# Optimization experiments

Hardware: AMD Instinct MI355X
Metric: run time of the kernel (lower is better)

## Reference

```python
import jax, jax.numpy as jnp
import numpy as np

N_NODES = 100000
N_EDGES = 1600000
N_GRAPHS = 1024
DIM_IN = 128
DIM_SF = 32
DIM_OUT = 8
EPS = 1e-5


def setup_inputs() -> dict:
    key = jax.random.key(0)
    ks = jax.random.split(key, 16)
    feat = jax.random.normal(ks[0], (N_NODES, DIM_IN), dtype=jnp.float32)
    self_feat = jax.random.normal(ks[1], (N_GRAPHS, DIM_SF), dtype=jnp.float32)
    src = jax.random.randint(ks[2], (N_EDGES,), 0, N_NODES)
    dst = jax.random.randint(ks[3], (N_EDGES,), 0, N_NODES)
    node2graph = jnp.sort(jax.random.randint(ks[4], (N_NODES,), 0, N_GRAPHS))

    def lin(k, din, dout):
        s = 1.0 / np.sqrt(din)
        kw, kb = jax.random.split(k)
        W = jax.random.uniform(kw, (din, dout), minval=-s, maxval=s, dtype=jnp.float32)
        b = jax.random.uniform(kb, (dout,), minval=-s, maxval=s, dtype=jnp.float32)
        return W, b

    W1, b1 = lin(ks[5], DIM_IN, 100)
    W2, b2 = lin(ks[6], 100, 20)
    Wf1, bf1 = lin(ks[7], 20 * DIM_SF, 128)
    Wf2, bf2 = lin(ks[8], 128, 32)
    Wf3, bf3 = lin(ks[9], 32, DIM_OUT)
    g1 = jnp.ones((128,), jnp.float32); be1 = jnp.zeros((128,), jnp.float32)
    g2 = jnp.ones((32,), jnp.float32); be2 = jnp.zeros((32,), jnp.float32)
    return dict(feat=feat, self_feat=self_feat, src=src, dst=dst,
                node2graph=node2graph, W1=W1, b1=b1, W2=W2, b2=b2,
                Wf1=Wf1, bf1=bf1, g1=g1, be1=be1,
                Wf2=Wf2, bf2=bf2, g2=g2, be2=be2, Wf3=Wf3, bf3=bf3)


def _gcn_layer(h, src, dst, W, b):
    # copy_u + mean reduce: segment-mean of source features onto destinations.
    n = h.shape[0]
    msum = jax.ops.segment_sum(h[src], dst, num_segments=n)        # [N, d]
    deg = jax.ops.segment_sum(jnp.ones((src.shape[0], 1), h.dtype), dst,
                              num_segments=n)                      # [N, 1]
    # DGL: nodes with no incoming messages keep their previous 'h'.
    agg = jnp.where(deg > 0, msum / jnp.maximum(deg, 1.0), h)
    return agg @ W + b


def _bn(x, gamma, beta):
    # BatchNorm1d in training mode: biased batch statistics.
    mu = jnp.mean(x, axis=0)
    var = jnp.mean((x - mu) ** 2, axis=0)
    return (x - mu) / jnp.sqrt(var + EPS) * gamma + beta


def reference(feat, self_feat, src, dst, node2graph,
              W1, b1, W2, b2, Wf1, bf1, g1, be1, Wf2, bf2, g2, be2, Wf3, bf3):
    h = jax.nn.relu(_gcn_layer(feat, src, dst, W1, b1))            # [N, 100]
    h = jax.nn.relu(_gcn_layer(h, src, dst, W2, b2))               # [N, 20]
    # dgl.mean_nodes: per-graph mean pooling
    hsum = jax.ops.segment_sum(h, node2graph, num_segments=N_GRAPHS)
    cnt = jax.ops.segment_sum(jnp.ones((h.shape[0], 1), h.dtype), node2graph,
                              num_segments=N_GRAPHS)
    hg = hsum / jnp.maximum(cnt, 1.0)                              # [G, 20]
    # Kronecker fusion: bmm(hg[:, :, None], self_feat[:, None, :])
    fused = (hg[:, :, None] * self_feat[:, None, :]).reshape(hg.shape[0], -1)
    out = jax.nn.relu(_bn(fused @ Wf1 + bf1, g1, be1))
    out = jax.nn.relu(_bn(out @ Wf2 + bf2, g2, be2))
    return out @ Wf3 + bf3                                         # [G, 8]
```

## Files before the change

### kernel.cpp

```cpp
#include <hip/hip_runtime.h>
#include <hip/hip_fp16.h>

#define N_NODES 100000
#define N_EDGES 1600000
#define N_GRAPHS 1024
#define DIM_IN 128
#define D1 100
#define D1P 128
#define D2 20
#define D2P 32
#define DIM_SF 32
#define DF1 128
#define DF2 32
#define DOUT 8
#define EPS 1e-5f
#define NPW 8

typedef _Float16 hh2 __attribute__((ext_vector_type(2)));

__device__ __forceinline__ void fdacc(unsigned u, float& lo, float& hi) {
  const hh2 MLO = {(_Float16)1.0f, (_Float16)0.0f};
  const hh2 MHI = {(_Float16)0.0f, (_Float16)1.0f};
  hh2 h = __builtin_bit_cast(hh2, u);
  lo = __builtin_amdgcn_fdot2(h, MLO, lo, false);
  hi = __builtin_amdgcn_fdot2(h, MHI, hi, false);
}

__device__ __forceinline__ unsigned pkadd(unsigned a, unsigned b) {
  __half2 x = __builtin_bit_cast(__half2, a);
  __half2 y = __builtin_bit_cast(__half2, b);
  return __builtin_bit_cast(unsigned, __hadd2(x, y));
}

#define NBK 512
#define BW 196
#define EPB 4096
#define NBLK1 ((N_EDGES + EPB - 1) / EPB)
#define GEMM1_NB (N_NODES / 80)

__global__ void __launch_bounds__(256) k_goff(const int* __restrict__ n2g,
                                              int* __restrict__ g_off,
                                              int* __restrict__ bucket_cnt) {
  int g = blockIdx.x * 256 + threadIdx.x;
  if (g < NBK) bucket_cnt[g] = 0;
  if (g > N_GRAPHS) return;
  if (g == N_GRAPHS) { g_off[g] = N_NODES; return; }
  int lo = 0, hi = N_NODES;
  while (lo < hi) {
    int mid = (lo + hi) >> 1;
    if (n2g[mid] < g) lo = mid + 1; else hi = mid;
  }
  g_off[g] = lo;
}

__global__ void __launch_bounds__(256) k_sc_gemm(const int* __restrict__ src,
                                                 const int* __restrict__ dst,
                                                 int* __restrict__ bucket_cnt,
                                                 unsigned* __restrict__ packed_out,
                                                 const float* __restrict__ feat,
                                                 const float* __restrict__ W1,
                                                 __half* __restrict__ p1h) {
  __shared__ __align__(16) char smem[31744];
  int t = threadIdx.x;
  if (blockIdx.x < NBLK1) {
    int* hist   = (int*)smem;
    int* lbase  = (int*)(smem + 2048);
    int* gbase  = (int*)(smem + 4096);
    int* ssum   = (int*)(smem + 6144);
    unsigned* sval = (unsigned*)(smem + 7168);
    unsigned short* sbkt = (unsigned short*)(smem + 23552);
    int blk = blockIdx.x;
    for (int i = t; i < NBK; i += 256) hist[i] = 0;
    __syncthreads();
    int base = blk * EPB;
    unsigned pk[16]; int bn[16]; int rk[16];
#pragma unroll
    for (int r = 0; r < 16; r++) {
      int e = base + r * 256 + t;
      bn[r] = -1;
      if (e < N_EDGES) {
        int dv = dst[e];
        unsigned b = (unsigned)dv / BW;
        unsigned ld = (unsigned)dv - b * BW;
        bn[r] = (int)b;
        pk[r] = ((unsigned)src[e] << 8) | ld;
        rk[r] = atomicAdd(&hist[b], 1);
      }
    }
    __syncthreads();
    int h0 = hist[2 * t], h1 = hist[2 * t + 1];
    int s = h0 + h1;
    ssum[t] = s; __syncthreads();
    for (int off = 1; off < 256; off <<= 1) {
      int x = (t >= off) ? ssum[t - off] : 0;
      __syncthreads();
      ssum[t] += x;
      __syncthreads();
    }
    int excl = ssum[t] - s;
    lbase[2 * t] = excl;
    lbase[2 * t + 1] = excl + h0;
    gbase[2 * t]     = (h0 > 0) ? (2 * t) * EPB     + atomicAdd(&bucket_cnt[2 * t],     h0) : 0;
    gbase[2 * t + 1] = (h1 > 0) ? (2 * t + 1) * EPB + atomicAdd(&bucket_cnt[2 * t + 1], h1) : 0;
    __syncthreads();
#pragma unroll
    for (int r = 0; r < 16; r++) {
      if (bn[r] >= 0) {
        int li = lbase[bn[r]] + rk[r];
        sval[li] = pk[r];
        sbkt[li] = (unsigned short)bn[r];
      }
    }
    __syncthreads();
    int cnt = N_EDGES - base; if (cnt > EPB) cnt = EPB;
    for (int i = t; i < cnt; i += 256) {
      int b = sbkt[i];
      packed_out[gbase[b] + (i - lbase[b])] = sval[i];
    }
  } else {
    float* w1s = (float*)smem;
    bool act = (t < 250);
    int q = t % 25, ng = t / 25;
    int n0 = (int)(blockIdx.x - NBLK1) * 80 + ng * 8;
    int c0 = q * 4;
    float acc[8][4] = {{0.f}};
    const float* f0 = feat + (size_t)n0 * DIM_IN;
    for (int pass = 0; pass < 2; pass++) {
      __syncthreads();
      for (int i = t; i < 64 * D1; i += 256) w1s[i] = W1[pass * 64 * D1 + i];
      __syncthreads();
      if (act) {
        int kg0 = pass * 64;
        for (int k = 0; k < 64; k += 4) {
          float4 w0 = *(const float4*)&w1s[(k + 0) * D1 + c0];
          float4 w1 = *(const float4*)&w1s[(k + 1) * D1 + c0];
          float4 w2 = *(const float4*)&w1s[(k + 2) * D1 + c0];
          float4 w3 = *(const float4*)&w1s[(k + 3) * D1 + c0];
#pragma unroll
          for (int j = 0; j < 8; j++) {
            float4 f = *(const float4*)(f0 + j * DIM_IN + kg0 + k);
            acc[j][0] += f.x * w0.x + f.y * w1.x + f.z * w2.x + f.w * w3.x;
            acc[j][1] += f.x * w0.y + f.y * w1.y + f.z * w2.y + f.w * w3.y;
            acc[j][2] += f.x * w0.z + f.y * w1.z + f.z * w2.z + f.w * w3.z;
            acc[j][3] += f.x * w0.w + f.y * w1.w + f.z * w2.w + f.w * w3.w;
          }
        }
      }
    }
    if (act) {
#pragma unroll
      for (int j = 0; j < 8; j++) {
        __half2* d2 = (__half2*)(p1h + (size_t)(n0 + j) * D1P + c0);
        d2[0] = __floats2half2_rn(acc[j][0], acc[j][1]);
        d2[1] = __floats2half2_rn(acc[j][2], acc[j][3]);
      }
    }
  }
}

__global__ void __launch_bounds__(256) k_bfine(const unsigned* __restrict__ packed_in,
                                               const int* __restrict__ bucket_cnt,
                                               int* __restrict__ csr,
                                               int* __restrict__ deg,
                                               int* __restrict__ row_off) {
  __shared__ unsigned sval[EPB];
  __shared__ int scsr[EPB];
  __shared__ int hist[256];
  __shared__ int soff[256];
  __shared__ int cur[256];
  int b = blockIdx.x, t = threadIdx.x;
  int start = b * EPB;
  int cnt = bucket_cnt[b];
  if (cnt > EPB) cnt = EPB;
  hist[t] = 0;
  __syncthreads();
  for (int i = t; i < cnt; i += 256) {
    unsigned v = packed_in[start + i];
    sval[i] = v;
    atomicAdd(&hist[v & 255u], 1);
  }
  __syncthreads();
  int h = hist[t];
  soff[t] = h; __syncthreads();
  for (int off = 1; off < 256; off <<= 1) {
    int x = (t >= off) ? soff[t - off] : 0;
    __syncthreads();
    soff[t] += x;
    __syncthreads();
  }
  int excl = soff[t] - h;
  cur[t] = excl;
  int n = b * BW + t;
  if (t < BW && n < N_NODES) { deg[n] = h; row_off[n] = start + excl; }
  __syncthreads();
  for (int i = t; i < cnt; i += 256) {
    unsigned v = sval[i];
    int pos = atomicAdd(&cur[v & 255u], 1);
    scsr[pos] = (int)(v >> 8);
  }
  __syncthreads();
  for (int i = t; i < cnt; i += 256) csr[start + i] = scsr[i];
}

__device__ __forceinline__ void acc8d(uint4 r, float4& A, float4& B) {
  fdacc(r.x, A.x, A.y);
  fdacc(r.y, A.z, A.w);
  fdacc(r.z, B.x, B.y);
  fdacc(r.w, B.z, B.w);
}

__global__ void __launch_bounds__(256) k_agg1(const __half* __restrict__ p1h,
                                              const int* __restrict__ deg,
                                              const int* __restrict__ row_off,
                                              const int* __restrict__ csr,
                                              const float* __restrict__ b1,
                                              const float* __restrict__ W2,
                                              __half* __restrict__ p2h) {
  __shared__ float w2s[D1 * D2];
  __shared__ float b1s[D1];
  __shared__ float hbuf[4][104];
  int t = threadIdx.x;
  for (int i = t; i < D1 * D2; i += 256) w2s[i] = W2[i];
  if (t < D1) b1s[t] = b1[t];
  __syncthreads();
  int w = t >> 6, lane = t & 63;
  int g = lane >> 4, o = lane & 15;
  const size_t oh = (size_t)(o * 8);
  int p = lane / 20;
  int j20 = lane - p * 20;
  int cbeg = (p == 0) ? 0 : (p == 1) ? 33 : 66;
  int cend = (p == 0) ? 33 : (p == 1) ? 66 : 100;
  if (p >= 3) { cbeg = 0; cend = 0; }
  int n0 = (blockIdx.x * 4 + w) * NPW;
  for (int nn = 0; nn < NPW; nn++) {
    int n = n0 + nn;
    int d = deg[n], ro = row_off[n];
    float4 A = {0.f, 0.f, 0.f, 0.f}, B = {0.f, 0.f, 0.f, 0.f};
    if (d > 0) {
      for (int base = 0; base < d; base += 64) {
        int m = d - base; if (m > 64) m = 64;
        int sv = (lane < m) ? csr[ro + base + lane] : 0;
        int nr = m >> 2;
        int r = 0;
        for (; r + 3 < nr; r += 4) {
          int sA = __shfl(sv, r * 4 + g);
          int sB = __shfl(sv, r * 4 + 4 + g);
          int sC = __shfl(sv, r * 4 + 8 + g);
          int sD = __shfl(sv, r * 4 + 12 + g);
          uint4 ra = *(const uint4*)(p1h + (size_t)sA * D1P + oh);
          uint4 rb = *(const uint4*)(p1h + (size_t)sB * D1P + oh);
          uint4 rc = *(const uint4*)(p1h + (size_t)sC * D1P + oh);
          uint4 rd = *(const uint4*)(p1h + (size_t)sD * D1P + oh);
          uint4 u, v2;
          u.x = pkadd(ra.x, rb.x); u.y = pkadd(ra.y, rb.y);
          u.z = pkadd(ra.z, rb.z); u.w = pkadd(ra.w, rb.w);
          v2.x = pkadd(rc.x, rd.x); v2.y = pkadd(rc.y, rd.y);
          v2.z = pkadd(rc.z, rd.z); v2.w = pkadd(rc.w, rd.w);
          acc8d(u, A, B);
          acc8d(v2, A, B);
        }
        if (r + 1 < nr) {
          int sA = __shfl(sv, r * 4 + g);
          int sB = __shfl(sv, r * 4 + 4 + g);
          uint4 ra = *(const uint4*)(p1h + (size_t)sA * D1P + oh);
          uint4 rb = *(const uint4*)(p1h + (size_t)sB * D1P + oh);
          uint4 u;
          u.x = pkadd(ra.x, rb.x); u.y = pkadd(ra.y, rb.y);
          u.z = pkadd(ra.z, rb.z); u.w = pkadd(ra.w, rb.w);
          acc8d(u, A, B);
          r += 2;
        }
        if (r < nr) {
          int sA = __shfl(sv, r * 4 + g);
          uint4 ra = *(const uint4*)(p1h + (size_t)sA * D1P + oh);
          acc8d(ra, A, B);
        }
        int rem = m & 3;
        int sT = __shfl(sv, nr * 4 + g);
        if (rem && g < rem) {
          uint4 ra = *(const uint4*)(p1h + (size_t)sT * D1P + oh);
          acc8d(ra, A, B);
        }
      }
    } else {
      if (g == 0) {
        uint4 ra = *(const uint4*)(p1h + (size_t)n * D1P + oh);
        acc8d(ra, A, B);
      }
    }
    float v[8] = {A.x, A.y, A.z, A.w, B.x, B.y, B.z, B.w};
#pragma unroll
    for (int j = 0; j < 8; j++) {
      v[j] += __shfl_down(v[j], 32);
      v[j] += __shfl_down(v[j], 16);
    }
    if (lane < 13) {
      float inv = (d > 0) ? 1.0f / (float)d : 1.0f;
#pragma unroll
      for (int j = 0; j < 8; j++) {
        int ch = 8 * lane + j;
        if (ch < D1) hbuf[w][ch] = fmaxf(v[j] * inv + b1s[ch], 0.f);
      }
    }
    float acc = 0.f;
    for (int c = cbeg; c < cend; c++) acc += hbuf[w][c] * w2s[c * D2 + j20];
    float t1 = __shfl_down(acc, 20);
    float t2 = __shfl_down(acc, 40);
    acc += t1 + t2;
    if (lane < D2)       p2h[(size_t)n * D2P + lane] = __float2half_rn(acc);
    else if (lane < D2P) p2h[(size_t)n * D2P + lane] = __float2half_rn(0.f);
  }
}

__global__ void __launch_bounds__(512) k_agg2(const __half* __restrict__ p2h,
                                              const int* __restrict__ deg,
                                              const int* __restrict__ row_off,
                                              const int* __restrict__ csr,
                                              const float* __restrict__ b2,
                                              const int* __restrict__ g_off,
                                              float* __restrict__ hg) {
  __shared__ float ssum[D2];
  __shared__ float b2s[D2];
  int t = threadIdx.x, w = t >> 6, lane = t & 63;
  int g = blockIdx.x;
  if (t < D2) { ssum[t] = 0.f; b2s[t] = b2[t]; }
  __syncthreads();
  const unsigned* pu = (const unsigned*)p2h;
  int n_lo = g_off[g], n_hi = g_off[g + 1];
  int nn = n_hi - n_lo;
  int e16 = lane >> 2, o = lane & 3;
  bool xtra = (o == 0);
  float4 GA = {0.f, 0.f, 0.f, 0.f};
  float4 GX = {0.f, 0.f, 0.f, 0.f};
  for (int n = n_lo + w; n < n_hi; n += 8) {
    int d = deg[n], ro = row_off[n];
    float4 A = {0.f, 0.f, 0.f, 0.f};
    float4 X = {0.f, 0.f, 0.f, 0.f};
    if (d > 0) {
      for (int base = 0; base < d; base += 64) {
        int m = d - base; if (m > 64) m = 64;
        int sv = (lane < m) ? csr[ro + base + lane] : 0;
        int nr = (m + 15) >> 4;
        for (int r = 0; r < nr; r++) {
          int ei = r * 16 + e16;
          int s0 = __shfl(sv, ei);
          if (ei < m) {
            const unsigned* row = pu + (size_t)s0 * 16;
            uint2 ra = *(const uint2*)(row + 2 * o);
            fdacc(ra.x, A.x, A.y);
            fdacc(ra.y, A.z, A.w);
            if (xtra) {
              uint2 rx = *(const uint2*)(row + 8);
              fdacc(rx.x, X.x, X.y);
              fdacc(rx.y, X.z, X.w);
            }
          }
        }
      }
    } else {
      if (e16 == 0) {
        const unsigned* row = pu + (size_t)n * 16;
        uint2 ra = *(const uint2*)(row + 2 * o);
        fdacc(ra.x, A.x, A.y);
        fdacc(ra.y, A.z, A.w);
        if (xtra) {
          uint2 rx = *(const uint2*)(row + 8);
          fdacc(rx.x, X.x, X.y);
          fdacc(rx.y, X.z, X.w);
        }
      }
    }
#pragma unroll
    for (int sft = 32; sft >= 4; sft >>= 1) {
      A.x += __shfl_down(A.x, sft); A.y += __shfl_down(A.y, sft);
      A.z += __shfl_down(A.z, sft); A.w += __shfl_down(A.w, sft);
      X.x += __shfl_down(X.x, sft); X.y += __shfl_down(X.y, sft);
      X.z += __shfl_down(X.z, sft); X.w += __shfl_down(X.w, sft);
    }
    float inv = (d > 0) ? 1.0f / (float)d : 1.0f;
    if (lane < 4) {
      int ch = 4 * lane;
      GA.x += fmaxf(A.x * inv + b2s[ch + 0], 0.f);
      GA.y += fmaxf(A.y * inv + b2s[ch + 1], 0.f);
      GA.z += fmaxf(A.z * inv + b2s[ch + 2], 0.f);
      GA.w += fmaxf(A.w * inv + b2s[ch + 3], 0.f);
      if (lane == 0) {
        GX.x += fmaxf(X.x * inv + b2s[16], 0.f);
        GX.y += fmaxf(X.y * inv + b2s[17], 0.f);
        GX.z += fmaxf(X.z * inv + b2s[18], 0.f);
        GX.w += fmaxf(X.w * inv + b2s[19], 0.f);
      }
    }
  }
  if (lane < 4) {
    int ch = 4 * lane;
    atomicAdd(&ssum[ch + 0], GA.x);
    atomicAdd(&ssum[ch + 1], GA.y);
    atomicAdd(&ssum[ch + 2], GA.z);
    atomicAdd(&ssum[ch + 3], GA.w);
    if (lane == 0) {
      atomicAdd(&ssum[16], GX.x);
      atomicAdd(&ssum[17], GX.y);
      atomicAdd(&ssum[18], GX.z);
      atomicAdd(&ssum[19], GX.w);
    }
  }
  __syncthreads();
  if (t < D2) {
    float inv = (nn > 0) ? 1.0f / (float)nn : 0.f;
    hg[g * D2 + t] = ssum[t] * inv;
  }
}

__global__ void __launch_bounds__(128) k_mlp1(const float* __restrict__ hg,
                                              const float* __restrict__ sf,
                                              const float* __restrict__ Wf1,
                                              const float* __restrict__ bf1,
                                              float* __restrict__ y1) {
  __shared__ float prod[D2 * DIM_SF];
  __shared__ float hgl[D2], sfl[DIM_SF];
  int g = blockIdx.x, t = threadIdx.x;
  if (t < D2) hgl[t] = hg[g * D2 + t];
  if (t < DIM_SF) sfl[t] = sf[g * DIM_SF + t];
  __syncthreads();
  for (int i = t; i < D2 * DIM_SF; i += 128) prod[i] = hgl[i >> 5] * sfl[i & 31];
  __syncthreads();
  float acc = bf1[t];
#pragma unroll 4
  for (int k = 0; k < D2 * DIM_SF; k++) acc += prod[k] * Wf1[k * DF1 + t];
  y1[g * DF1 + t] = acc;
}

__global__ void k_bnstats(const float* __restrict__ x, int ld,
                          float* __restrict__ mu, float* __restrict__ rstd) {
  __shared__ float ssum[256], ssq[256];
  int c = blockIdx.x, t = threadIdx.x;
  float s = 0.f, q = 0.f;
  for (int r = t; r < N_GRAPHS; r += 256) { float v = x[r * ld + c]; s += v; q += v * v; }
  ssum[t] = s; ssq[t] = q; __syncthreads();
  for (int off = 128; off > 0; off >>= 1) {
    if (t < off) { ssum[t] += ssum[t + off]; ssq[t] += ssq[t + off]; }
    __syncthreads();
  }
  if (t == 0) {
    float m = ssum[0] / (float)N_GRAPHS;
    float var = ssq[0] / (float)N_GRAPHS - m * m;
    mu[c] = m;
    rstd[c] = rsqrtf(var + EPS);
  }
}

__global__ void k_mlp2(const float* __restrict__ y1, const float* __restrict__ mu1,
                       const float* __restrict__ rstd1, const float* __restrict__ g1,
                       const float* __restrict__ be1, const float* __restrict__ Wf2,
                       const float* __restrict__ bf2, float* __restrict__ y2) {
  int idx = blockIdx.x * 256 + threadIdx.x;
  int g = idx >> 5, o = idx & 31;
  float acc = bf2[o];
  for (int k = 0; k < DF1; k++) {
    float x = (y1[g * DF1 + k] - mu1[k]) * rstd1[k] * g1[k] + be1[k];
    x = fmaxf(x, 0.f);
    acc += x * Wf2[k * DF2 + o];
  }
  y2[g * DF2 + o] = acc;
}

__global__ void k_mlp3(const float* __restrict__ y2, const float* __restrict__ mu2,
                       const float* __restrict__ rstd2, const float* __restrict__ g2,
                       const float* __restrict__ be2, const float* __restrict__ Wf3,
                       const float* __restrict__ bf3, float* __restrict__ out) {
  int idx = blockIdx.x * 256 + threadIdx.x;
  int g = idx >> 3, o = idx & 7;
  float acc = bf3[o];
  for (int k = 0; k < DF2; k++) {
    float x = (y2[g * DF2 + k] - mu2[k]) * rstd2[k] * g2[k] + be2[k];
    x = fmaxf(x, 0.f);
    acc += x * Wf3[k * DOUT + o];
  }
  out[g * DOUT + o] = acc;
}

extern "C" void kernel_launch(void* const* d_in, const int* in_sizes, int n_in,
                              void* d_out, int out_size, void* d_ws, size_t ws_size,
                              hipStream_t stream) {
  const float* feat = (const float*)d_in[0];
  const float* sf   = (const float*)d_in[1];
  const int*   src  = (const int*)d_in[2];
  const int*   dst  = (const int*)d_in[3];
  const int*   n2g  = (const int*)d_in[4];
  const float* W1   = (const float*)d_in[5];
  const float* b1   = (const float*)d_in[6];
  const float* W2   = (const float*)d_in[7];
  const float* b2   = (const float*)d_in[8];
  const float* Wf1  = (const float*)d_in[9];
  const float* bf1  = (const float*)d_in[10];
  const float* g1   = (const float*)d_in[11];
  const float* be1  = (const float*)d_in[12];
  const float* Wf2  = (const float*)d_in[13];
  const float* bf2  = (const float*)d_in[14];
  const float* g2   = (const float*)d_in[15];
  const float* be2  = (const float*)d_in[16];
  const float* Wf3  = (const float*)d_in[17];
  const float* bf3  = (const float*)d_in[18];
  float* out = (float*)d_out;

  char* ws = (char*)d_ws;
  size_t off = 0;
  auto alloc = [&](size_t bytes) -> void* {
    void* p = ws + off;
    off = (off + bytes + 255) & ~(size_t)255;
    return p;
  };
  int*      bucket_cnt = (int*)alloc(NBK * 4);
  int*      g_offs   = (int*)alloc((N_GRAPHS + 1) * 4);
  float*    hg       = (float*)alloc(N_GRAPHS * D2 * 4);
  int*      deg      = (int*)alloc(N_NODES * 4);
  int*      row_off  = (int*)alloc(N_NODES * 4);
  unsigned* packed   = (unsigned*)alloc((size_t)NBK * EPB * 4);
  int*      csr      = (int*)alloc((size_t)NBK * EPB * 4);
  __half*   p1h      = (__half*)alloc((size_t)N_NODES * D1P * 2);
  __half*   p2h      = (__half*)alloc((size_t)N_NODES * D2P * 2);
  float*    y1       = (float*)alloc((size_t)N_GRAPHS * DF1 * 4);
  float*    y2       = (float*)alloc((size_t)N_GRAPHS * DF2 * 4);
  float*    mu1      = (float*)alloc(DF1 * 4);
  float*    rstd1    = (float*)alloc(DF1 * 4);
  float*    mu2      = (float*)alloc(DF2 * 4);
  float*    rstd2    = (float*)alloc(DF2 * 4);

  k_goff<<<(N_GRAPHS + 1 + 255) / 256, 256, 0, stream>>>(n2g, g_offs, bucket_cnt);
  k_sc_gemm<<<NBLK1 + GEMM1_NB, 256, 0, stream>>>(src, dst, bucket_cnt, packed,
                                                  feat, W1, p1h);
  k_bfine<<<NBK, 256, 0, stream>>>(packed, bucket_cnt, csr, deg, row_off);
  k_agg1<<<N_NODES / (4 * NPW), 256, 0, stream>>>(p1h, deg, row_off, csr, b1, W2, p2h);
  k_agg2<<<N_GRAPHS, 512, 0, stream>>>(p2h, deg, row_off, csr, b2, g_offs, hg);
  k_mlp1<<<N_GRAPHS, 128, 0, stream>>>(hg, sf, Wf1, bf1, y1);
  k_bnstats<<<DF1, 256, 0, stream>>>(y1, DF1, mu1, rstd1);
  k_mlp2<<<(N_GRAPHS * DF2) / 256, 256, 0, stream>>>(y1, mu1, rstd1, g1, be1, Wf2, bf2, y2);
  k_bnstats<<<DF2, 256, 0, stream>>>(y2, DF2, mu2, rstd2);
  k_mlp3<<<(N_GRAPHS * DOUT) / 256, 256, 0, stream>>>(y2, mu2, rstd2, g2, be2, Wf3, bf3, out);
}
```

Measured before the change: 403.6 us.

## Fuse first MLP layer into graph pooling kernel and halve scatter block size

```diff
diff --git a/kernel.cpp b/kernel.cpp
--- a/kernel.cpp
+++ b/kernel.cpp
@@ -34,7 +34,8 @@
 
 #define NBK 512
 #define BW 196
-#define EPB 4096
+#define BKCAP 4096
+#define EPB 2048
 #define NBLK1 ((N_EDGES + EPB - 1) / EPB)
 #define GEMM1_NB (N_NODES / 80)
 
@@ -60,7 +61,7 @@
                                                  const float* __restrict__ feat,
                                                  const float* __restrict__ W1,
                                                  __half* __restrict__ p1h) {
-  __shared__ __align__(16) char smem[31744];
+  __shared__ __align__(16) char smem[19456];
   int t = threadIdx.x;
   if (blockIdx.x < NBLK1) {
     int* hist   = (int*)smem;
@@ -68,14 +69,14 @@
     int* gbase  = (int*)(smem + 4096);
     int* ssum   = (int*)(smem + 6144);
     unsigned* sval = (unsigned*)(smem + 7168);
-    unsigned short* sbkt = (unsigned short*)(smem + 23552);
+    unsigned short* sbkt = (unsigned short*)(smem + 15360);
     int blk = blockIdx.x;
     for (int i = t; i < NBK; i += 256) hist[i] = 0;
     __syncthreads();
     int base = blk * EPB;
-    unsigned pk[16]; int bn[16]; int rk[16];
-#pragma unroll
-    for (int r = 0; r < 16; r++) {
+    unsigned pk[8]; int bn[8]; int rk[8];
+#pragma unroll
+    for (int r = 0; r < 8; r++) {
       int e = base + r * 256 + t;
       bn[r] = -1;
       if (e < N_EDGES) {
@@ -100,11 +101,11 @@
     int excl = ssum[t] - s;
     lbase[2 * t] = excl;
     lbase[2 * t + 1] = excl + h0;
-    gbase[2 * t]     = (h0 > 0) ? (2 * t) * EPB     + atomicAdd(&bucket_cnt[2 * t],     h0) : 0;
-    gbase[2 * t + 1] = (h1 > 0) ? (2 * t + 1) * EPB + atomicAdd(&bucket_cnt[2 * t + 1], h1) : 0;
-    __syncthreads();
-#pragma unroll
-    for (int r = 0; r < 16; r++) {
+    gbase[2 * t]     = (h0 > 0) ? (2 * t) * BKCAP     + atomicAdd(&bucket_cnt[2 * t],     h0) : 0;
+    gbase[2 * t + 1] = (h1 > 0) ? (2 * t + 1) * BKCAP + atomicAdd(&bucket_cnt[2 * t + 1], h1) : 0;
+    __syncthreads();
+#pragma unroll
+    for (int r = 0; r < 8; r++) {
       if (bn[r] >= 0) {
         int li = lbase[bn[r]] + rk[r];
         sval[li] = pk[r];
@@ -125,13 +126,13 @@
     int c0 = q * 4;
     float acc[8][4] = {{0.f}};
     const float* f0 = feat + (size_t)n0 * DIM_IN;
-    for (int pass = 0; pass < 2; pass++) {
+    for (int pass = 0; pass < 4; pass++) {
       __syncthreads();
-      for (int i = t; i < 64 * D1; i += 256) w1s[i] = W1[pass * 64 * D1 + i];
+      for (int i = t; i < 32 * D1; i += 256) w1s[i] = W1[pass * 32 * D1 + i];
       __syncthreads();
       if (act) {
-        int kg0 = pass * 64;
-        for (int k = 0; k < 64; k += 4) {
+        int kg0 = pass * 32;
+        for (int k = 0; k < 32; k += 4) {
           float4 w0 = *(const float4*)&w1s[(k + 0) * D1 + c0];
           float4 w1 = *(const float4*)&w1s[(k + 1) * D1 + c0];
           float4 w2 = *(const float4*)&w1s[(k + 2) * D1 + c0];
@@ -163,15 +164,15 @@
                                                int* __restrict__ csr,
                                                int* __restrict__ deg,
                                                int* __restrict__ row_off) {
-  __shared__ unsigned sval[EPB];
-  __shared__ int scsr[EPB];
+  __shared__ unsigned sval[BKCAP];
+  __shared__ int scsr[BKCAP];
   __shared__ int hist[256];
   __shared__ int soff[256];
   __shared__ int cur[256];
   int b = blockIdx.x, t = threadIdx.x;
-  int start = b * EPB;
+  int start = b * BKCAP;
   int cnt = bucket_cnt[b];
-  if (cnt > EPB) cnt = EPB;
+  if (cnt > BKCAP) cnt = BKCAP;
   hist[t] = 0;
   __syncthreads();
   for (int i = t; i < cnt; i += 256) {
@@ -318,12 +319,19 @@
                                               const int* __restrict__ csr,
                                               const float* __restrict__ b2,
                                               const int* __restrict__ g_off,
-                                              float* __restrict__ hg) {
+                                              const float* __restrict__ sf,
+                                              const float* __restrict__ Wf1,
+                                              const float* __restrict__ bf1,
+                                              float* __restrict__ y1) {
   __shared__ float ssum[D2];
   __shared__ float b2s[D2];
+  __shared__ float hgl[D2], sfl[DIM_SF];
+  __shared__ float prod[D2 * DIM_SF];
+  __shared__ float red[512];
   int t = threadIdx.x, w = t >> 6, lane = t & 63;
   int g = blockIdx.x;
   if (t < D2) { ssum[t] = 0.f; b2s[t] = b2[t]; }
+  if (t < DIM_SF) sfl[t] = sf[g * DIM_SF + t];
   __syncthreads();
   const unsigned* pu = (const unsigned*)p2h;
   int n_lo = g_off[g], n_hi = g_off[g + 1];
@@ -408,27 +416,22 @@
   __syncthreads();
   if (t < D2) {
     float inv = (nn > 0) ? 1.0f / (float)nn : 0.f;
-    hg[g * D2 + t] = ssum[t] * inv;
-  }
-}
-
-__global__ void __launch_bounds__(128) k_mlp1(const float* __restrict__ hg,
-                                              const float* __restrict__ sf,
-                                              const float* __restrict__ Wf1,
-                                              const float* __restrict__ bf1,
-                                              float* __restrict__ y1) {
-  __shared__ float prod[D2 * DIM_SF];
-  __shared__ float hgl[D2], sfl[DIM_SF];
-  int g = blockIdx.x, t = threadIdx.x;
-  if (t < D2) hgl[t] = hg[g * D2 + t];
-  if (t < DIM_SF) sfl[t] = sf[g * DIM_SF + t];
-  __syncthreads();
-  for (int i = t; i < D2 * DIM_SF; i += 128) prod[i] = hgl[i >> 5] * sfl[i & 31];
-  __syncthreads();
-  float acc = bf1[t];
+    hgl[t] = ssum[t] * inv;
+  }
+  __syncthreads();
+  for (int i = t; i < D2 * DIM_SF; i += 512) prod[i] = hgl[i >> 5] * sfl[i & 31];
+  __syncthreads();
+  {
+    int col = t & 127, qq = t >> 7;
+    float part = 0.f;
+    int k0 = qq * 160;
 #pragma unroll 4
-  for (int k = 0; k < D2 * DIM_SF; k++) acc += prod[k] * Wf1[k * DF1 + t];
-  y1[g * DF1 + t] = acc;
+    for (int k = k0; k < k0 + 160; k++) part += prod[k] * Wf1[k * DF1 + col];
+    red[t] = part;
+    __syncthreads();
+    if (t < DF1)
+      y1[g * DF1 + t] = bf1[t] + ((red[t] + red[t + 128]) + (red[t + 256] + red[t + 384]));
+  }
 }
 
 __global__ void k_bnstats(const float* __restrict__ x, int ld,
@@ -513,11 +516,10 @@
   };
   int*      bucket_cnt = (int*)alloc(NBK * 4);
   int*      g_offs   = (int*)alloc((N_GRAPHS + 1) * 4);
-  float*    hg       = (float*)alloc(N_GRAPHS * D2 * 4);
   int*      deg      = (int*)alloc(N_NODES * 4);
   int*      row_off  = (int*)alloc(N_NODES * 4);
-  unsigned* packed   = (unsigned*)alloc((size_t)NBK * EPB * 4);
-  int*      csr      = (int*)alloc((size_t)NBK * EPB * 4);
+  unsigned* packed   = (unsigned*)alloc((size_t)NBK * BKCAP * 4);
+  int*      csr      = (int*)alloc((size_t)NBK * BKCAP * 4);
   __half*   p1h      = (__half*)alloc((size_t)N_NODES * D1P * 2);
   __half*   p2h      = (__half*)alloc((size_t)N_NODES * D2P * 2);
   float*    y1       = (float*)alloc((size_t)N_GRAPHS * DF1 * 4);
@@ -532,8 +534,8 @@
                                                   feat, W1, p1h);
   k_bfine<<<NBK, 256, 0, stream>>>(packed, bucket_cnt, csr, deg, row_off);
   k_agg1<<<N_NODES / (4 * NPW), 256, 0, stream>>>(p1h, deg, row_off, csr, b1, W2, p2h);
-  k_agg2<<<N_GRAPHS, 512, 0, stream>>>(p2h, deg, row_off, csr, b2, g_offs, hg);
-  k_mlp1<<<N_GRAPHS, 128, 0, stream>>>(hg, sf, Wf1, bf1, y1);
+  k_agg2<<<N_GRAPHS, 512, 0, stream>>>(p2h, deg, row_off, csr, b2, g_offs,
+                                       sf, Wf1, bf1, y1);
   k_bnstats<<<DF1, 256, 0, stream>>>(y1, DF1, mu1, rstd1);
   k_mlp2<<<(N_GRAPHS * DF2) / 256, 256, 0, stream>>>(y1, mu1, rstd1, g1, be1, Wf2, bf2, y2);
   k_bnstats<<<DF2, 256, 0, stream>>>(y2, DF2, mu2, rstd2);
```

New measurement: 397.7 us. Within noise of the previous version (-1.5%).
